# Performance work log

Hardware: AMD Instinct MI355X
Metric: run time of the kernel (lower is better)

## Reference

```python
import jax, jax.numpy as jnp
import numpy as np
from jax import lax

D_MODEL = 192
D_STATE = 16
D_CONV = 4
EXPAND = 2
D_INNER = D_MODEL * EXPAND           # 384
DT_RANK = (D_MODEL + 15) // 16       # 12
B, H, W = 4, 32, 32
N = H * W                            # 1024


def layernorm(x, g, b, eps=1e-5):
    m = x.mean(-1, keepdims=True)
    v = ((x - m) ** 2).mean(-1, keepdims=True)
    return (x - m) / jnp.sqrt(v + eps) * g + b


def mamba(u, Win, cw, cb, Wxp, Wdt, bdt, Alog, Dp, Wout):
    """mamba-ssm Mamba block. u: (B, L, d_model)."""
    Bb, L, _ = u.shape
    xz = u @ Win.T                                  # (B,L,2*d_inner)
    xh, z = jnp.split(xz, 2, axis=-1)
    # causal depthwise conv1d
    xc = xh.transpose(0, 2, 1)                      # (B,d_inner,L)
    xc = lax.conv_general_dilated(
        xc, cw[:, None, :], (1,), [(D_CONV - 1, 0)],
        feature_group_count=D_INNER,
        dimension_numbers=('NCH', 'OIH', 'NCH')) + cb[None, :, None]
    xs = jax.nn.silu(xc).transpose(0, 2, 1)         # (B,L,d_inner)
    dbl = xs @ Wxp.T                                # (B,L,dt_rank+2*d_state)
    dt = dbl[..., :DT_RANK]
    Bm = dbl[..., DT_RANK:DT_RANK + D_STATE]
    Cm = dbl[..., DT_RANK + D_STATE:]
    dt = jax.nn.softplus(dt @ Wdt.T + bdt)          # (B,L,d_inner)
    A = -jnp.exp(Alog)                              # (d_inner,d_state)

    def step(h, inp):
        dt_t, B_t, C_t, x_t = inp                   # (B,di),(B,ds),(B,ds),(B,di)
        dA = jnp.exp(dt_t[..., None] * A)           # (B,di,ds)
        h = dA * h + dt_t[..., None] * B_t[:, None, :] * x_t[..., None]
        return h, jnp.einsum('bds,bs->bd', h, C_t)

    h0 = jnp.zeros((Bb, D_INNER, D_STATE), u.dtype)
    _, ys = lax.scan(step, h0, (dt.transpose(1, 0, 2), Bm.transpose(1, 0, 2),
                                Cm.transpose(1, 0, 2), xs.transpose(1, 0, 2)))
    y = ys.transpose(1, 0, 2) + xs * Dp
    y = y * jax.nn.silu(z)
    return y @ Wout.T


mamba4 = jax.vmap(mamba)  # batched over the 4 scan directions


def to_col(x):    # row-major -> column-major sequence order
    return x.reshape(-1, H, W, D_MODEL).transpose(0, 2, 1, 3).reshape(-1, N, D_MODEL)


def from_col(x):  # inverse of to_col
    return x.reshape(-1, W, H, D_MODEL).transpose(0, 2, 1, 3).reshape(-1, N, D_MODEL)


def setup_inputs() -> dict:
    key = jax.random.key(0)
    ks = iter(jax.random.split(key, 32))
    s = 0.02
    d, di, ds, r = D_MODEL, D_INNER, D_STATE, DT_RANK
    inp = {}
    inp['x'] = jax.random.normal(next(ks), (B, d, H, W), jnp.float32)
    inp['norm_g'] = jnp.ones((d,), jnp.float32)
    inp['norm_b'] = jnp.zeros((d,), jnp.float32)
    inp['in_w'] = jax.random.normal(next(ks), (d, d), jnp.float32) * s
    inp['in_b'] = jnp.zeros((d,), jnp.float32)
    # 4 stacked Mamba blocks
    inp['m_in_w'] = jax.random.normal(next(ks), (4, 2 * di, d), jnp.float32) * s
    inp['m_conv_w'] = jax.random.normal(next(ks), (4, di, D_CONV), jnp.float32) * s
    inp['m_conv_b'] = jnp.zeros((4, di), jnp.float32)
    inp['m_xp_w'] = jax.random.normal(next(ks), (4, r + 2 * ds, di), jnp.float32) * s
    inp['m_dt_w'] = jax.random.normal(next(ks), (4, di, r), jnp.float32) * s
    inp['m_dt_b'] = jax.random.normal(next(ks), (4, di), jnp.float32) * 0.1 - 4.0
    inp['m_Alog'] = jnp.log(jnp.tile(jnp.arange(1, ds + 1, dtype=jnp.float32), (4, di, 1)))
    inp['m_D'] = jnp.ones((4, di), jnp.float32)
    inp['m_out_w'] = jax.random.normal(next(ks), (4, d, di), jnp.float32) * s
    # fusion MLP
    inp['f_w1'] = jax.random.normal(next(ks), (2 * d, 4 * d), jnp.float32) * s
    inp['f_b1'] = jnp.zeros((2 * d,), jnp.float32)
    inp['f_w2'] = jax.random.normal(next(ks), (d, 2 * d), jnp.float32) * s
    inp['f_b2'] = jnp.zeros((d,), jnp.float32)
    inp['o_w'] = jax.random.normal(next(ks), (d, d), jnp.float32) * s
    inp['o_b'] = jnp.zeros((d,), jnp.float32)
    inp['on_g'] = jnp.ones((d,), jnp.float32)
    inp['on_b'] = jnp.zeros((d,), jnp.float32)
    return inp


def reference(x, norm_g, norm_b, in_w, in_b, m_in_w, m_conv_w, m_conv_b,
              m_xp_w, m_dt_w, m_dt_b, m_Alog, m_D, m_out_w,
              f_w1, f_b1, f_w2, f_b2, o_w, o_b, on_g, on_b):
    xs = x.reshape(B, D_MODEL, N).transpose(0, 2, 1)     # b c h w -> b (hw) c
    xs = layernorm(xs, norm_g, norm_b)
    xp = xs @ in_w.T + in_b
    col = to_col(xp)
    seqs = jnp.stack([xp, jnp.flip(xp, 1), col, jnp.flip(col, 1)], 0)  # (4,B,N,C)
    ys = mamba4(seqs, m_in_w, m_conv_w, m_conv_b, m_xp_w, m_dt_w, m_dt_b,
                m_Alog, m_D, m_out_w)
    o0 = ys[0]
    o1 = jnp.flip(ys[1], 1)
    o2 = from_col(ys[2])
    o3 = from_col(jnp.flip(ys[3], 1))
    fused = jnp.concatenate([o0, o1, o2, o3], -1)        # (B,N,4C)
    hdn = jax.nn.gelu(fused @ f_w1.T + f_b1, approximate=False)
    hdn = hdn @ f_w2.T + f_b2
    out = hdn @ o_w.T + o_b
    out = layernorm(out, on_g, on_b) + xs
    return out.transpose(0, 2, 1).reshape(B, D_MODEL, H, W)
```

## Files before the change

kernel.cpp:

```cpp
#include <hip/hip_runtime.h>
#include <cstddef>

#define DM 192
#define DI 384
#define DS 16
#define DR 12
#define L 1024
#define ROWS 4096
#define SEG 32
#define ST  32

typedef unsigned short ushortx;
typedef short bf16x8 __attribute__((ext_vector_type(8)));
typedef float f32x4  __attribute__((ext_vector_type(4)));

__device__ __forceinline__ float wave_sum(float v) {
  #pragma unroll
  for (int off = 32; off > 0; off >>= 1) v += __shfl_xor(v, off);
  return v;
}

__device__ __forceinline__ ushortx f2bf(float x) {
  unsigned u = __float_as_uint(x);
  u += 0x7fffu + ((u >> 16) & 1u);
  return (ushortx)(u >> 16);
}
__device__ __forceinline__ float bf2f(ushortx u) {
  return __uint_as_float(((unsigned)u) << 16);
}

__device__ __forceinline__ int map_row(int t, int mode) {
  switch (mode) {
    case 1: return 1023 - t;
    case 2: return ((t & 31) << 5) | (t >> 5);
    case 3: { int u = 1023 - t; return ((u & 31) << 5) | (u >> 5); }
    case 4: return 1023 - (((t & 31) << 5) | (t >> 5));
    default: return t;
  }
}

struct WcvtArgs {
  const float* src[6];
  unsigned int off[6];
  unsigned int n[6];
};
__global__ __launch_bounds__(256) void prep_kernel(
    WcvtArgs a, ushortx* __restrict__ dst,
    const float* __restrict__ in_w, unsigned int_off,
    const float* __restrict__ in_b, float* __restrict__ bC,
    const float* __restrict__ x, const float* __restrict__ g,
    const float* __restrict__ b, float* __restrict__ xs, ushortx* __restrict__ xs_bf)
{
  int y = blockIdx.y;
  if (y < 6) {
    int i = (blockIdx.x * 256 + threadIdx.x) * 4;
    if (i < (int)a.n[y]) {
      float4 v = *(const float4*)(a.src[y] + i);
      ushort4 o;
      o.x = f2bf(v.x); o.y = f2bf(v.y); o.z = f2bf(v.z); o.w = f2bf(v.w);
      *(ushort4*)(dst + a.off[y] + i) = o;
    }
    return;
  }
  if (y == 6) {
    int i = blockIdx.x * 256 + threadIdx.x;
    if (i < DM * DM) {
      int n = i / DM, j = i % DM;
      dst[int_off + i] = f2bf(in_w[(size_t)j * DM + n]);
    }
    return;
  }
  if (y == 8) {
    int idx = blockIdx.x * 256 + threadIdx.x;
    if (idx < 4 * 768) {
      int k = idx / 768, n = idx % 768;
      const float* wr = a.src[0] + (size_t)k * 768 * DM + (size_t)n * DM;
      float acc = 0.f;
      for (int j = 0; j < DM; ++j) acc = fmaf(wr[j], in_b[j], acc);
      bC[idx] = acc;
    }
    return;
  }
  if (blockIdx.x >= 1024) return;
  int wave = threadIdx.x >> 6;
  int lane = threadIdx.x & 63;
  int r = blockIdx.x * 4 + wave;
  int bb = r >> 10, n = r & 1023;
  const float* xb = x + (size_t)bb * DM * L + n;
  float v[3];
  float s = 0.f, s2 = 0.f;
  #pragma unroll
  for (int j = 0; j < 3; ++j) {
    int c = lane + j * 64;
    v[j] = xb[(size_t)c * L];
    s += v[j]; s2 += v[j] * v[j];
  }
  s = wave_sum(s); s2 = wave_sum(s2);
  float mean = s * (1.f / DM);
  float var  = s2 * (1.f / DM) - mean * mean;
  float rstd = rsqrtf(var + 1e-5f);
  float* xo = xs + (size_t)r * DM;
  ushortx* xob = xs_bf + (size_t)r * DM;
  #pragma unroll
  for (int j = 0; j < 3; ++j) {
    int c = lane + j * 64;
    float val = (v[j] - mean) * rstd * g[c] + b[c];
    xo[c] = val;
    xob[c] = f2bf(val);
  }
}

template <int NIT>
__global__ __launch_bounds__(256) void gemm_fullk_kernel(
    const ushortx* __restrict__ A, int lda, const ushortx* __restrict__ W,
    const float* __restrict__ bias, ushortx* __restrict__ Cb,
    int ldc, int coff, int4 perm,
    long astride, long wstride, long cstride, int coffstride, int bstride)
{
  __shared__ __align__(16) short As[2][64][40];
  __shared__ __align__(16) short Bs[2][64][40];

  int z = blockIdx.z;
  A += (size_t)z * astride;
  W += (size_t)z * wstride;
  Cb += (size_t)z * cstride;
  if (bias) bias += (size_t)z * bstride;
  int permMode = (z == 0) ? perm.x : (z == 1) ? perm.y : (z == 2) ? perm.z : perm.w;
  int co = coff + z * coffstride;
  const int K = NIT * 32;

  int tid = threadIdx.x;
  int m0 = blockIdx.x * 64;
  int n0 = blockIdx.y * 64;

  int ar = tid >> 2, ak = (tid & 3) * 8;
  int arow = m0 + ar;
  int amrow = (arow & ~1023) | map_row(arow & 1023, permMode);
  const ushortx* ap = A + (size_t)amrow * lda + ak;
  const ushortx* wp = W + (size_t)(n0 + ar) * K + ak;

  int lane = tid & 63;
  int w = tid >> 6, wm = w >> 1, wn = w & 1;
  int lm = lane & 15, lq = lane >> 4;

  bf16x8 rA[NIT], rB[NIT];
  #pragma unroll
  for (int ki = 0; ki < NIT; ++ki) rA[ki] = *(const bf16x8*)(ap + ki * 32);
  #pragma unroll
  for (int ki = 0; ki < NIT; ++ki) rB[ki] = *(const bf16x8*)(wp + ki * 32);

  f32x4 acc[2][2];
  #pragma unroll
  for (int i = 0; i < 2; ++i)
    #pragma unroll
    for (int j = 0; j < 2; ++j) acc[i][j] = (f32x4){0.f, 0.f, 0.f, 0.f};

  *(bf16x8*)&As[0][ar][ak] = rA[0];
  *(bf16x8*)&Bs[0][ar][ak] = rB[0];
  __syncthreads();

  #pragma unroll
  for (int ki = 0; ki < NIT; ++ki) {
    int cur = ki & 1;
    bf16x8 fa[2], fb[2];
    #pragma unroll
    for (int i = 0; i < 2; ++i)
      fa[i] = *(const bf16x8*)&As[cur][wm * 32 + i * 16 + lm][lq * 8];
    #pragma unroll
    for (int j = 0; j < 2; ++j)
      fb[j] = *(const bf16x8*)&Bs[cur][wn * 32 + j * 16 + lm][lq * 8];
    #pragma unroll
    for (int i = 0; i < 2; ++i)
      #pragma unroll
      for (int j = 0; j < 2; ++j)
        acc[i][j] = __builtin_amdgcn_mfma_f32_16x16x32_bf16(fa[i], fb[j], acc[i][j], 0, 0, 0);
    if (ki + 1 < NIT) {
      int nxt = cur ^ 1;
      *(bf16x8*)&As[nxt][ar][ak] = rA[ki + 1];
      *(bf16x8*)&Bs[nxt][ar][ak] = rB[ki + 1];
      __syncthreads();
    }
  }

  #pragma unroll
  for (int i = 0; i < 2; ++i) {
    #pragma unroll
    for (int r = 0; r < 4; ++r) {
      int row = m0 + wm * 32 + i * 16 + lq * 4 + r;
      #pragma unroll
      for (int j = 0; j < 2; ++j) {
        int n = n0 + wn * 32 + j * 16 + lm;
        float v = acc[i][j][r];
        if (bias) v += bias[n];
        Cb[(size_t)row * ldc + co + n] = f2bf(v);
      }
    }
  }
}

template <int BM, int BN>
__global__ __launch_bounds__(256) void gemm_kernel(
    const ushortx* __restrict__ A, int lda, const ushortx* __restrict__ W,
    const float* __restrict__ bias, float* __restrict__ C, ushortx* __restrict__ Cb,
    int N, int K, int ldc, int coff, int4 perm, int act,
    long astride, long wstride, long cstride, int coffstride, int bstride)
{
  constexpr int MF = BM / 32;
  constexpr int NF = BN / 32;
  constexpr int AR = (BM * 32) / (256 * 8);
  constexpr int BR = (BN * 32) / (256 * 8);
  __shared__ __align__(16) short As[2][BM][40];
  __shared__ __align__(16) short Bs[2][BN][40];

  int z = blockIdx.z;
  A += (size_t)z * astride;
  W += (size_t)z * wstride;
  if (C)  C  += (size_t)z * cstride;
  if (Cb) Cb += (size_t)z * cstride;
  if (bias) bias += (size_t)z * bstride;
  int permMode = (z == 0) ? perm.x : (z == 1) ? perm.y : (z == 2) ? perm.z : perm.w;
  int co = coff + z * coffstride;

  int tid = threadIdx.x;
  int m0 = blockIdx.x * BM;
  int n0 = blockIdx.y * BN;

  int ar, ak;
  if (AR == 2) { ar = tid >> 1; ak = (tid & 1) * 16; }
  else         { ar = tid >> 2; ak = (tid & 3) * 8; }
  int arow = m0 + ar;
  int amrow = (arow & ~1023) | map_row(arow & 1023, permMode);
  const ushortx* ap = A + (size_t)amrow * lda + ak;

  int bn, bk;
  if (BR == 2) { bn = tid >> 1; bk = (tid & 1) * 16; }
  else         { bn = tid >> 2; bk = (tid & 3) * 8; }
  const ushortx* wp = W + (size_t)(n0 + bn) * K + bk;
  bool bok = (n0 + bn) < N;

  int lane = tid & 63;
  int w = tid >> 6, wm = w >> 1, wn = w & 1;
  int lm = lane & 15, lq = lane >> 4;

  f32x4 acc[MF][NF];
  #pragma unroll
  for (int i = 0; i < MF; ++i)
    #pragma unroll
    for (int j = 0; j < NF; ++j) acc[i][j] = (f32x4){0.f, 0.f, 0.f, 0.f};

  const bf16x8 zz = {0, 0, 0, 0, 0, 0, 0, 0};
  bf16x8 ra[AR], rb[BR];

  #pragma unroll
  for (int u = 0; u < AR; ++u) ra[u] = *(const bf16x8*)(ap + u * 8);
  #pragma unroll
  for (int u = 0; u < BR; ++u) rb[u] = bok ? *(const bf16x8*)(wp + u * 8) : zz;
  #pragma unroll
  for (int u = 0; u < AR; ++u) *(bf16x8*)&As[0][ar][ak + u * 8] = ra[u];
  #pragma unroll
  for (int u = 0; u < BR; ++u) *(bf16x8*)&Bs[0][bn][bk + u * 8] = rb[u];
  __syncthreads();

  int niter = K >> 5;
  for (int ki = 0; ki < niter; ++ki) {
    int cur = ki & 1;
    if (ki + 1 < niter) {
      int k0 = (ki + 1) * 32;
      #pragma unroll
      for (int u = 0; u < AR; ++u) ra[u] = *(const bf16x8*)(ap + k0 + u * 8);
      #pragma unroll
      for (int u = 0; u < BR; ++u) rb[u] = bok ? *(const bf16x8*)(wp + k0 + u * 8) : zz;
    }
    bf16x8 fa[MF], fb[NF];
    #pragma unroll
    for (int i = 0; i < MF; ++i)
      fa[i] = *(const bf16x8*)&As[cur][wm * (BM / 2) + i * 16 + lm][lq * 8];
    #pragma unroll
    for (int j = 0; j < NF; ++j)
      fb[j] = *(const bf16x8*)&Bs[cur][wn * (BN / 2) + j * 16 + lm][lq * 8];
    #pragma unroll
    for (int i = 0; i < MF; ++i)
      #pragma unroll
      for (int j = 0; j < NF; ++j)
        acc[i][j] = __builtin_amdgcn_mfma_f32_16x16x32_bf16(fa[i], fb[j], acc[i][j], 0, 0, 0);
    if (ki + 1 < niter) {
      int nxt = cur ^ 1;
      #pragma unroll
      for (int u = 0; u < AR; ++u) *(bf16x8*)&As[nxt][ar][ak + u * 8] = ra[u];
      #pragma unroll
      for (int u = 0; u < BR; ++u) *(bf16x8*)&Bs[nxt][bn][bk + u * 8] = rb[u];
      __syncthreads();
    }
  }

  #pragma unroll
  for (int i = 0; i < MF; ++i) {
    #pragma unroll
    for (int r = 0; r < 4; ++r) {
      int row = m0 + wm * (BM / 2) + i * 16 + lq * 4 + r;
      #pragma unroll
      for (int j = 0; j < NF; ++j) {
        int n = n0 + wn * (BN / 2) + j * 16 + lm;
        if (n < N) {
          float v = acc[i][j][r];
          if (bias) v += bias[n];
          if (act == 1) v = 0.5f * v * (1.f + erff(v * 0.70710678118f));
          if (C)  C [(size_t)row * ldc + co + n] = v;
          if (Cb) Cb[(size_t)row * ldc + co + n] = f2bf(v);
        }
      }
    }
  }
}

__global__ __launch_bounds__(256) void gemm_ln_kernel(
    const ushortx* __restrict__ A, const ushortx* __restrict__ W,
    const float* __restrict__ ob, const float* __restrict__ g,
    const float* __restrict__ b, const float* __restrict__ xs,
    float* __restrict__ out)
{
  __shared__ __align__(16) char smem[64 * 200 * 4];
  short* As0 = (short*)smem;
  short* As1 = As0 + 64 * 40;
  short* Bs0 = As1 + 64 * 40;
  short* Bs1 = Bs0 + 192 * 40;
  float* Ct  = (float*)smem;

  int tid = threadIdx.x;
  int m0 = blockIdx.x * 64;

  int ar = tid >> 2, ak = (tid & 3) * 8;
  const ushortx* ap = A + (size_t)(m0 + ar) * DM + ak;

  int lane = tid & 63;
  int w = tid >> 6, wm = w >> 1, wn = w & 1;
  int lm = lane & 15, lq = lane >> 4;

  f32x4 acc[2][6];
  #pragma unroll
  for (int i = 0; i < 2; ++i)
    #pragma unroll
    for (int j = 0; j < 6; ++j) acc[i][j] = (f32x4){0.f, 0.f, 0.f, 0.f};

  bf16x8 ra, rb[3];
  ra = *(const bf16x8*)ap;
  #pragma unroll
  for (int u = 0; u < 3; ++u) {
    int c = tid + u * 256;
    rb[u] = *(const bf16x8*)(W + (size_t)(c >> 2) * DM + (c & 3) * 8);
  }
  *(bf16x8*)&As0[ar * 40 + ak] = ra;
  #pragma unroll
  for (int u = 0; u < 3; ++u) {
    int c = tid + u * 256;
    *(bf16x8*)&Bs0[(c >> 2) * 40 + (c & 3) * 8] = rb[u];
  }
  __syncthreads();

  const int niter = DM / 32;
  for (int ki = 0; ki < niter; ++ki) {
    short* Ac = (ki & 1) ? As1 : As0;
    short* Bc = (ki & 1) ? Bs1 : Bs0;
    if (ki + 1 < niter) {
      int k0 = (ki + 1) * 32;
      ra = *(const bf16x8*)(ap + k0);
      #pragma unroll
      for (int u = 0; u < 3; ++u) {
        int c = tid + u * 256;
        rb[u] = *(const bf16x8*)(W + (size_t)(c >> 2) * DM + (c & 3) * 8 + k0);
      }
    }
    bf16x8 fa[2], fb[6];
    #pragma unroll
    for (int i = 0; i < 2; ++i)
      fa[i] = *(const bf16x8*)&Ac[(wm * 32 + i * 16 + lm) * 40 + lq * 8];
    #pragma unroll
    for (int j = 0; j < 6; ++j)
      fb[j] = *(const bf16x8*)&Bc[(wn * 96 + j * 16 + lm) * 40 + lq * 8];
    #pragma unroll
    for (int i = 0; i < 2; ++i)
      #pragma unroll
      for (int j = 0; j < 6; ++j)
        acc[i][j] = __builtin_amdgcn_mfma_f32_16x16x32_bf16(fa[i], fb[j], acc[i][j], 0, 0, 0);
    if (ki + 1 < niter) {
      short* An = (ki & 1) ? As0 : As1;
      short* Bn = (ki & 1) ? Bs0 : Bs1;
      *(bf16x8*)&An[ar * 40 + ak] = ra;
      #pragma unroll
      for (int u = 0; u < 3; ++u) {
        int c = tid + u * 256;
        *(bf16x8*)&Bn[(c >> 2) * 40 + (c & 3) * 8] = rb[u];
      }
    }
    __syncthreads();
  }

  #pragma unroll
  for (int i = 0; i < 2; ++i) {
    #pragma unroll
    for (int r = 0; r < 4; ++r) {
      int row = wm * 32 + i * 16 + lq * 4 + r;
      #pragma unroll
      for (int j = 0; j < 6; ++j) {
        int col = wn * 96 + j * 16 + lm;
        Ct[row * 200 + col] = acc[i][j][r] + ob[col];
      }
    }
  }
  __syncthreads();

  int row = tid >> 2, p = tid & 3;
  const float* base = Ct + row * 200 + p * 48;
  float s = 0.f, s2 = 0.f;
  #pragma unroll
  for (int c = 0; c < 48; ++c) { float v = base[c]; s += v; s2 += v * v; }
  s  += __shfl_xor(s, 1);  s  += __shfl_xor(s, 2);
  s2 += __shfl_xor(s2, 1); s2 += __shfl_xor(s2, 2);
  float mean = s * (1.f / DM);
  float var  = s2 * (1.f / DM) - mean * mean;
  float rstd = rsqrtf(var + 1e-5f);
  int gr = m0 + row, bb = gr >> 10, n = gr & 1023;
  const float* xsr = xs + (size_t)gr * DM + p * 48;
  float* op = out + (size_t)bb * DM * L + n;
  #pragma unroll
  for (int c48 = 0; c48 < 48; ++c48) {
    int c = p * 48 + c48;
    float val = (base[c48] - mean) * rstd * g[c] + b[c] + xsr[c48];
    op[(size_t)c * L] = val;
  }
}

__global__ __launch_bounds__(256) void conv_silu_kernel(
    const ushortx* __restrict__ xz, const float* __restrict__ cw,
    const float* __restrict__ cb, ushortx* __restrict__ xsm_bf)
{
  int idx = blockIdx.x * 256 + threadIdx.x;
  int d = idx % DI;
  int rest = idx / DI;
  int tq = rest & 255;
  int seq = rest >> 8;
  int k = seq >> 2;
  int t0 = tq * 4;
  const ushortx* xh = xz + (size_t)seq * L * (2 * DI) + d;
  const float* w = cw + ((size_t)k * DI + d) * 4;
  float w0 = w[0], w1 = w[1], w2 = w[2], w3 = w[3];
  float bias = cb[k * DI + d];
  float in[7];
  #pragma unroll
  for (int j = 0; j < 7; ++j) {
    int t = t0 - 3 + j;
    in[j] = (t >= 0) ? bf2f(xh[(size_t)t * (2 * DI)]) : 0.f;
  }
  ushortx* yo = xsm_bf + ((size_t)seq * L + t0) * DI + d;
  #pragma unroll
  for (int i = 0; i < 4; ++i) {
    float acc = bias;
    acc = fmaf(w0, in[i],     acc);
    acc = fmaf(w1, in[i + 1], acc);
    acc = fmaf(w2, in[i + 2], acc);
    acc = fmaf(w3, in[i + 3], acc);
    float sig = 1.f / (1.f + __expf(-acc));
    yo[(size_t)i * DI] = f2bf(acc * sig);
  }
}

__global__ __launch_bounds__(256) void dt_kernel(
    const float* __restrict__ dbl, const float* __restrict__ Wdt,
    const float* __restrict__ bdt, ushortx* __restrict__ dt)
{
  int idx = blockIdx.x * 256 + threadIdx.x;
  int d = idx % DI;
  int row = idx / DI;
  int k = row >> 12;
  const float* dl = dbl + (size_t)row * 44;
  const float* w = Wdt + ((size_t)k * DI + d) * DR;
  float acc = bdt[k * DI + d];
  #pragma unroll
  for (int r = 0; r < DR; ++r) acc = fmaf(w[r], dl[r], acc);
  float v = (acc > 20.f) ? acc : log1pf(__expf(acc));
  dt[idx] = f2bf(v);
}

__global__ __launch_bounds__(64) void scan_pass1(
    const float* __restrict__ dbl, const ushortx* __restrict__ dt,
    const ushortx* __restrict__ xsm_bf, const float* __restrict__ Alog,
    float* __restrict__ hseg, float* __restrict__ Sseg)
{
  __shared__ __align__(16) float sB[ST][16];
  int seq = blockIdx.y, g = blockIdx.z, k = seq >> 2;
  int d = blockIdx.x * 64 + threadIdx.x;

  const float* bbase = dbl + ((size_t)seq * L + g * ST) * 44 + 12;
  #pragma unroll
  for (int j = 0; j < 2; ++j) {
    int i = threadIdx.x + j * 64;
    int t = i >> 2, q = (i & 3) * 4;
    *(float4*)&sB[t][q] = *(const float4*)(bbase + (size_t)t * 44 + q);
  }
  float A[16];
  const float* alp = Alog + ((size_t)k * DI + d) * DS;
  #pragma unroll
  for (int s = 0; s < 16; ++s) A[s] = -__expf(alp[s]);

  const ushortx* dtp = dt     + ((size_t)seq * L + g * ST) * DI + d;
  const ushortx* xp  = xsm_bf + ((size_t)seq * L + g * ST) * DI + d;
  __syncthreads();

  float h[16];
  #pragma unroll
  for (int s = 0; s < 16; ++s) h[s] = 0.f;
  float sdt = 0.f;
  float rDt[4], rX[4];
  #pragma unroll
  for (int j = 0; j < 4; ++j) {
    rDt[j] = bf2f(dtp[(size_t)j * DI]);
    rX [j] = bf2f(xp [(size_t)j * DI]);
  }

  #pragma unroll 4
  for (int t = 0; t < ST; ++t) {
    float dtv = rDt[t & 3], xv = rX[t & 3];
    if (t + 4 < ST) {
      rDt[t & 3] = bf2f(dtp[(size_t)(t + 4) * DI]);
      rX [t & 3] = bf2f(xp [(size_t)(t + 4) * DI]);
    }
    float dtx = dtv * xv;
    sdt += dtv;
    #pragma unroll
    for (int s = 0; s < 16; ++s) {
      float dA = __expf(dtv * A[s]);
      h[s] = fmaf(dA, h[s], dtx * sB[t][s]);
    }
  }
  float* hp = hseg + (((size_t)seq * SEG + g) * DI + d) * DS;
  #pragma unroll
  for (int s = 0; s < 16; ++s) hp[s] = h[s];
  Sseg[((size_t)seq * SEG + g) * DI + d] = sdt;
}

__global__ __launch_bounds__(64) void scan_mid(
    float* __restrict__ hseg, const float* __restrict__ Sseg,
    const float* __restrict__ Alog)
{
  int seq = blockIdx.y, k = seq >> 2;
  int d = blockIdx.x * 64 + threadIdx.x;
  float A[16];
  const float* alp = Alog + ((size_t)k * DI + d) * DS;
  #pragma unroll
  for (int s = 0; s < 16; ++s) A[s] = -__expf(alp[s]);
  float h[16];
  #pragma unroll
  for (int s = 0; s < 16; ++s) h[s] = 0.f;
  for (int g = 0; g < SEG; ++g) {
    float* hp = hseg + (((size_t)seq * SEG + g) * DI + d) * DS;
    float Sg = Sseg[((size_t)seq * SEG + g) * DI + d];
    float tmp[16];
    #pragma unroll
    for (int s = 0; s < 16; ++s) tmp[s] = hp[s];
    #pragma unroll
    for (int s = 0; s < 16; ++s) hp[s] = h[s];
    #pragma unroll
    for (int s = 0; s < 16; ++s)
      h[s] = fmaf(h[s], __expf(A[s] * Sg), tmp[s]);
  }
}

__global__ __launch_bounds__(64) void scan_pass2(
    const float* __restrict__ dbl, const ushortx* __restrict__ dt,
    const ushortx* __restrict__ xz,
    ushortx* __restrict__ xy,
    const float* __restrict__ Alog, const float* __restrict__ Dp,
    const float* __restrict__ hseg)
{
  __shared__ __align__(16) float sBC[ST][32];
  int seq = blockIdx.y, g = blockIdx.z, k = seq >> 2;
  int d = blockIdx.x * 64 + threadIdx.x;

  const float* bcbase = dbl + ((size_t)seq * L + g * ST) * 44 + 12;
  #pragma unroll
  for (int j = 0; j < 4; ++j) {
    int i = threadIdx.x + j * 64;
    int t = i >> 3, q = (i & 7) * 4;
    *(float4*)&sBC[t][q] = *(const float4*)(bcbase + (size_t)t * 44 + q);
  }
  float A[16];
  const float* alp = Alog + ((size_t)k * DI + d) * DS;
  #pragma unroll
  for (int s = 0; s < 16; ++s) A[s] = -__expf(alp[s]);
  float Dv = Dp[k * DI + d];

  float h[16];
  {
    const float* hp = hseg + (((size_t)seq * SEG + g) * DI + d) * DS;
    #pragma unroll
    for (int s = 0; s < 16; ++s) h[s] = hp[s];
  }

  const ushortx* dtp = dt + ((size_t)seq * L + g * ST) * DI + d;
  const ushortx* zp  = xz + ((size_t)seq * L + g * ST) * (2 * DI) + DI + d;
  ushortx*       yp  = xy + ((size_t)seq * L + g * ST) * DI + d;
  __syncthreads();

  float rDt[4], rX[4], rZ[4];
  #pragma unroll
  for (int j = 0; j < 4; ++j) {
    rDt[j] = bf2f(dtp[(size_t)j * DI]);
    rX [j] = bf2f(yp [(size_t)j * DI]);
    rZ [j] = bf2f(zp [(size_t)j * (2 * DI)]);
  }

  #pragma unroll 4
  for (int t = 0; t < ST; ++t) {
    float dtv = rDt[t & 3], xv = rX[t & 3], zv = rZ[t & 3];
    if (t + 4 < ST) {
      rDt[t & 3] = bf2f(dtp[(size_t)(t + 4) * DI]);
      rX [t & 3] = bf2f(yp [(size_t)(t + 4) * DI]);
      rZ [t & 3] = bf2f(zp [(size_t)(t + 4) * (2 * DI)]);
    }
    float dtx = dtv * xv;
    float y = 0.f;
    #pragma unroll
    for (int s = 0; s < 16; ++s) {
      float dA = __expf(dtv * A[s]);
      h[s] = fmaf(dA, h[s], dtx * sBC[t][s]);
      y = fmaf(h[s], sBC[t][16 + s], y);
    }
    y = fmaf(Dv, xv, y);
    float sig = 1.f / (1.f + __expf(-zv));
    yp[(size_t)t * DI] = f2bf(y * (zv * sig));
  }
}

template <int BM, int BN>
static inline void gemm(const ushortx* A, int lda, const ushortx* W, const float* bias,
                        float* C, ushortx* Cb,
                        int N, int K, int ldc, int coff, int4 perm, int act,
                        int nz, long astride, long wstride, long cstride, int coffstride,
                        hipStream_t s, int M = ROWS, int bstride = 0) {
  dim3 grid(M / BM, (N + BN - 1) / BN, nz);
  gemm_kernel<BM, BN><<<grid, 256, 0, s>>>(A, lda, W, bias, C, Cb, N, K, ldc, coff, perm, act,
                                           astride, wstride, cstride, coffstride, bstride);
}

extern "C" void kernel_launch(void* const* d_in, const int* in_sizes, int n_in,
                              void* d_out, int out_size, void* d_ws, size_t ws_size,
                              hipStream_t stream) {
  (void)in_sizes; (void)n_in; (void)out_size; (void)ws_size;
  const float* x        = (const float*)d_in[0];
  const float* norm_g   = (const float*)d_in[1];
  const float* norm_b   = (const float*)d_in[2];
  const float* in_w     = (const float*)d_in[3];
  const float* in_b     = (const float*)d_in[4];
  const float* m_in_w   = (const float*)d_in[5];
  const float* m_conv_w = (const float*)d_in[6];
  const float* m_conv_b = (const float*)d_in[7];
  const float* m_xp_w   = (const float*)d_in[8];
  const float* m_dt_w   = (const float*)d_in[9];
  const float* m_dt_b   = (const float*)d_in[10];
  const float* m_Alog   = (const float*)d_in[11];
  const float* m_D      = (const float*)d_in[12];
  const float* m_out_w  = (const float*)d_in[13];
  const float* f_w1     = (const float*)d_in[14];
  const float* f_b1     = (const float*)d_in[15];
  const float* f_w2     = (const float*)d_in[16];
  const float* f_b2     = (const float*)d_in[17];
  const float* o_w      = (const float*)d_in[18];
  const float* o_b      = (const float*)d_in[19];
  const float* on_g     = (const float*)d_in[20];
  const float* on_b     = (const float*)d_in[21];
  float* out = (float*)d_out;

  float* ws   = (float*)d_ws;
  float* xs   = ws;
  float* dbl  = xs + 786432;
  float* hseg = dbl + 720896;
  float* Sseg = hseg + 3145728;
  float* bC   = Sseg + 196608;
  ushortx* xs_bf  = (ushortx*)(bC + 4096);
  ushortx* wbf    = xs_bf + 786432;
  ushortx* WinC   = wbf + 1394688;
  ushortx* dt_bf  = WinC + 589824;
  ushortx* xz_bf  = dt_bf + 6291456;
  ushortx* xsm_bf = xz_bf + 12582912;
  ushortx* fused_bf = xz_bf;
  ushortx* hdn_bf   = fused_bf + 3145728;
  ushortx* h2_bf    = hdn_bf + 1572864;

  const unsigned W_MIN = 0, W_XP = 589824, W_OUT = 657408, W_F1 = 952320,
                 W_F2 = 1247232, W_O = 1320960, W_INT = 1357824;

  int4 p0 = make_int4(0, 0, 0, 0);
  int4 pfwd = make_int4(0, 1, 2, 3);
  int4 pinv = make_int4(0, 1, 2, 4);

  {
    WcvtArgs a;
    a.src[0] = m_in_w;  a.off[0] = W_MIN; a.n[0] = 589824;
    a.src[1] = m_xp_w;  a.off[1] = W_XP;  a.n[1] = 67584;
    a.src[2] = m_out_w; a.off[2] = W_OUT; a.n[2] = 294912;
    a.src[3] = f_w1;    a.off[3] = W_F1;  a.n[3] = 294912;
    a.src[4] = f_w2;    a.off[4] = W_F2;  a.n[4] = 73728;
    a.src[5] = o_w;     a.off[5] = W_O;   a.n[5] = 36864;
    prep_kernel<<<dim3(1024, 9), 256, 0, stream>>>(
        a, wbf, in_w, W_INT, in_b, bC, x, norm_g, norm_b, xs, xs_bf);
  }
  gemm<64, 64>(wbf + W_MIN, DM, wbf + W_INT, nullptr, nullptr, WinC,
               DM, DM, DM, 0, p0, 0, 4, (long)768 * DM, 0, (long)768 * DM, 0,
               stream, 768);
  gemm_fullk_kernel<6><<<dim3(ROWS / 64, 768 / 64, 4), 256, 0, stream>>>(
      xs_bf, DM, WinC, bC, xz_bf, 2 * DI, 0, pfwd,
      0, (long)768 * DM, (long)ROWS * 2 * DI, 0, 768);
  conv_silu_kernel<<<(16 * 256 * DI) / 256, 256, 0, stream>>>(xz_bf, m_conv_w, m_conv_b, xsm_bf);
  gemm<64, 64>(xsm_bf, DI, wbf + W_XP, nullptr, dbl, nullptr, 44, DI, 44, 0, p0, 0,
               4, (long)ROWS * DI, (long)44 * DI, (long)ROWS * 44, 0, stream);
  dt_kernel<<<(16 * L * DI) / 256, 256, 0, stream>>>(dbl, m_dt_w, m_dt_b, dt_bf);
  scan_pass1<<<dim3(DI / 64, 16, SEG), 64, 0, stream>>>(dbl, dt_bf, xsm_bf, m_Alog, hseg, Sseg);
  scan_mid<<<dim3(DI / 64, 16), 64, 0, stream>>>(hseg, Sseg, m_Alog);
  scan_pass2<<<dim3(DI / 64, 16, SEG), 64, 0, stream>>>(dbl, dt_bf, xz_bf, xsm_bf,
                                                        m_Alog, m_D, hseg);
  gemm_fullk_kernel<12><<<dim3(ROWS / 64, DM / 64, 4), 256, 0, stream>>>(
      xsm_bf, DI, wbf + W_OUT, nullptr, fused_bf, 4 * DM, 0, pinv,
      (long)ROWS * DI, (long)DM * DI, 0, DM, 0);
  gemm<64, 64>(fused_bf, 4 * DM, wbf + W_F1, f_b1, nullptr, hdn_bf, 2 * DM, 4 * DM, 2 * DM,
               0, p0, 1, 1, 0, 0, 0, 0, stream);
  gemm_fullk_kernel<12><<<dim3(ROWS / 64, DM / 64, 1), 256, 0, stream>>>(
      hdn_bf, 2 * DM, wbf + W_F2, f_b2, h2_bf, DM, 0, p0,
      0, 0, 0, 0, 0);
  gemm_ln_kernel<<<64, 256, 0, stream>>>(h2_bf, wbf + W_O, o_b, on_g, on_b, xs, out);
}
```

Before: 298.3 us.

## Fuse dt projection into scan passes, parallelize scan_mid, shrink gemm_ln tiles

Removes the separate dt_kernel and recomputes the dt projection plus softplus inside both scan passes from the dbl rows staged in shared memory. This avoids writing and twice re-reading a bf16 dt tensor of 16x1024x384 elements, at the cost of twelve extra FMAs and a softplus per step in each pass. scan_mid is rewritten to assign one thread per (d, state) pair with prefetched loads, which raises parallelism for the serial segment combine. gemm_ln_kernel now uses 16-row tiles, giving 256 blocks instead of 64 and better GPU occupancy, though it re-reads the weight tile more often.

Result: slower. 311.1 us (+4.3%).

```diff
diff --git a/kernel.cpp b/kernel.cpp
--- a/kernel.cpp
+++ b/kernel.cpp
@@ -319,113 +319,102 @@
     const float* __restrict__ b, const float* __restrict__ xs,
     float* __restrict__ out)
 {
-  __shared__ __align__(16) char smem[64 * 200 * 4];
-  short* As0 = (short*)smem;
-  short* As1 = As0 + 64 * 40;
-  short* Bs0 = As1 + 64 * 40;
-  short* Bs1 = Bs0 + 192 * 40;
-  float* Ct  = (float*)smem;
+  __shared__ __align__(16) short As[2][16][40];
+  __shared__ __align__(16) short Bs[2][192][40];
+  __shared__ float Ct[16][200];
 
   int tid = threadIdx.x;
-  int m0 = blockIdx.x * 64;
-
-  int ar = tid >> 2, ak = (tid & 3) * 8;
+  int m0 = blockIdx.x * 16;
+
+  bool aok = tid < 64;
+  int ar = (tid >> 2) & 15, ak = (tid & 3) * 8;
   const ushortx* ap = A + (size_t)(m0 + ar) * DM + ak;
 
   int lane = tid & 63;
-  int w = tid >> 6, wm = w >> 1, wn = w & 1;
+  int w = tid >> 6;
   int lm = lane & 15, lq = lane >> 4;
 
-  f32x4 acc[2][6];
-  #pragma unroll
-  for (int i = 0; i < 2; ++i)
-    #pragma unroll
-    for (int j = 0; j < 6; ++j) acc[i][j] = (f32x4){0.f, 0.f, 0.f, 0.f};
+  f32x4 acc[3];
+  #pragma unroll
+  for (int j = 0; j < 3; ++j) acc[j] = (f32x4){0.f, 0.f, 0.f, 0.f};
 
   bf16x8 ra, rb[3];
-  ra = *(const bf16x8*)ap;
+  if (aok) ra = *(const bf16x8*)ap;
   #pragma unroll
   for (int u = 0; u < 3; ++u) {
     int c = tid + u * 256;
     rb[u] = *(const bf16x8*)(W + (size_t)(c >> 2) * DM + (c & 3) * 8);
   }
-  *(bf16x8*)&As0[ar * 40 + ak] = ra;
+  if (aok) *(bf16x8*)&As[0][ar][ak] = ra;
   #pragma unroll
   for (int u = 0; u < 3; ++u) {
     int c = tid + u * 256;
-    *(bf16x8*)&Bs0[(c >> 2) * 40 + (c & 3) * 8] = rb[u];
+    *(bf16x8*)&Bs[0][c >> 2][(c & 3) * 8] = rb[u];
   }
   __syncthreads();
 
   const int niter = DM / 32;
   for (int ki = 0; ki < niter; ++ki) {
-    short* Ac = (ki & 1) ? As1 : As0;
-    short* Bc = (ki & 1) ? Bs1 : Bs0;
+    int cur = ki & 1;
     if (ki + 1 < niter) {
       int k0 = (ki + 1) * 32;
-      ra = *(const bf16x8*)(ap + k0);
+      if (aok) ra = *(const bf16x8*)(ap + k0);
       #pragma unroll
       for (int u = 0; u < 3; ++u) {
         int c = tid + u * 256;
         rb[u] = *(const bf16x8*)(W + (size_t)(c >> 2) * DM + (c & 3) * 8 + k0);
       }
     }
-    bf16x8 fa[2], fb[6];
-    #pragma unroll
-    for (int i = 0; i < 2; ++i)
-      fa[i] = *(const bf16x8*)&Ac[(wm * 32 + i * 16 + lm) * 40 + lq * 8];
-    #pragma unroll
-    for (int j = 0; j < 6; ++j)
-      fb[j] = *(const bf16x8*)&Bc[(wn * 96 + j * 16 + lm) * 40 + lq * 8];
-    #pragma unroll
-    for (int i = 0; i < 2; ++i)
-      #pragma unroll
-      for (int j = 0; j < 6; ++j)
-        acc[i][j] = __builtin_amdgcn_mfma_f32_16x16x32_bf16(fa[i], fb[j], acc[i][j], 0, 0, 0);
+    bf16x8 fa = *(const bf16x8*)&As[cur][lm][lq * 8];
+    bf16x8 fb[3];
+    #pragma unroll
+    for (int j = 0; j < 3; ++j)
+      fb[j] = *(const bf16x8*)&Bs[cur][w * 48 + j * 16 + lm][lq * 8];
+    #pragma unroll
+    for (int j = 0; j < 3; ++j)
+      acc[j] = __builtin_amdgcn_mfma_f32_16x16x32_bf16(fa, fb[j], acc[j], 0, 0, 0);
     if (ki + 1 < niter) {
-      short* An = (ki & 1) ? As0 : As1;
-      short* Bn = (ki & 1) ? Bs0 : Bs1;
-      *(bf16x8*)&An[ar * 40 + ak] = ra;
+      int nxt = cur ^ 1;
+      if (aok) *(bf16x8*)&As[nxt][ar][ak] = ra;
       #pragma unroll
       for (int u = 0; u < 3; ++u) {
         int c = tid + u * 256;
-        *(bf16x8*)&Bn[(c >> 2) * 40 + (c & 3) * 8] = rb[u];
+        *(bf16x8*)&Bs[nxt][c >> 2][(c & 3) * 8] = rb[u];
       }
-    }
-    __syncthreads();
-  }
-
-  #pragma unroll
-  for (int i = 0; i < 2; ++i) {
-    #pragma unroll
-    for (int r = 0; r < 4; ++r) {
-      int row = wm * 32 + i * 16 + lq * 4 + r;
-      #pragma unroll
-      for (int j = 0; j < 6; ++j) {
-        int col = wn * 96 + j * 16 + lm;
-        Ct[row * 200 + col] = acc[i][j][r] + ob[col];
-      }
+      __syncthreads();
+    }
+  }
+
+  #pragma unroll
+  for (int r = 0; r < 4; ++r) {
+    int row = lq * 4 + r;
+    #pragma unroll
+    for (int j = 0; j < 3; ++j) {
+      int col = w * 48 + j * 16 + lm;
+      Ct[row][col] = acc[j][r] + ob[col];
     }
   }
   __syncthreads();
 
-  int row = tid >> 2, p = tid & 3;
-  const float* base = Ct + row * 200 + p * 48;
+  int row = tid >> 4, p = tid & 15;
+  const float* base = &Ct[row][0] + p * 12;
   float s = 0.f, s2 = 0.f;
   #pragma unroll
-  for (int c = 0; c < 48; ++c) { float v = base[c]; s += v; s2 += v * v; }
+  for (int c = 0; c < 12; ++c) { float v = base[c]; s += v; s2 += v * v; }
   s  += __shfl_xor(s, 1);  s  += __shfl_xor(s, 2);
+  s  += __shfl_xor(s, 4);  s  += __shfl_xor(s, 8);
   s2 += __shfl_xor(s2, 1); s2 += __shfl_xor(s2, 2);
+  s2 += __shfl_xor(s2, 4); s2 += __shfl_xor(s2, 8);
   float mean = s * (1.f / DM);
   float var  = s2 * (1.f / DM) - mean * mean;
   float rstd = rsqrtf(var + 1e-5f);
   int gr = m0 + row, bb = gr >> 10, n = gr & 1023;
-  const float* xsr = xs + (size_t)gr * DM + p * 48;
+  const float* xsr = xs + (size_t)gr * DM + p * 12;
   float* op = out + (size_t)bb * DM * L + n;
   #pragma unroll
-  for (int c48 = 0; c48 < 48; ++c48) {
-    int c = p * 48 + c48;
-    float val = (base[c48] - mean) * rstd * g[c] + b[c] + xsr[c48];
+  for (int c12 = 0; c12 < 12; ++c12) {
+    int c = p * 12 + c12;
+    float val = (base[c12] - mean) * rstd * g[c] + b[c] + xsr[c12];
     op[(size_t)c * L] = val;
   }
 }
@@ -464,72 +453,74 @@
   }
 }
 
-__global__ __launch_bounds__(256) void dt_kernel(
-    const float* __restrict__ dbl, const float* __restrict__ Wdt,
-    const float* __restrict__ bdt, ushortx* __restrict__ dt)
-{
-  int idx = blockIdx.x * 256 + threadIdx.x;
-  int d = idx % DI;
-  int row = idx / DI;
-  int k = row >> 12;
-  const float* dl = dbl + (size_t)row * 44;
-  const float* w = Wdt + ((size_t)k * DI + d) * DR;
-  float acc = bdt[k * DI + d];
-  #pragma unroll
-  for (int r = 0; r < DR; ++r) acc = fmaf(w[r], dl[r], acc);
-  float v = (acc > 20.f) ? acc : log1pf(__expf(acc));
-  dt[idx] = f2bf(v);
+__device__ __forceinline__ float dt_inline(const float* __restrict__ row,
+                                           const float wdt[12], float bdt_v) {
+  float a0 = fmaf(wdt[0], row[0], bdt_v);
+  float a1 = wdt[1] * row[1];
+  float a2 = wdt[2] * row[2];
+  float a3 = wdt[3] * row[3];
+  #pragma unroll
+  for (int r = 4; r < 12; r += 4) {
+    a0 = fmaf(wdt[r],     row[r],     a0);
+    a1 = fmaf(wdt[r + 1], row[r + 1], a1);
+    a2 = fmaf(wdt[r + 2], row[r + 2], a2);
+    a3 = fmaf(wdt[r + 3], row[r + 3], a3);
+  }
+  float acc = (a0 + a1) + (a2 + a3);
+  return (acc > 20.f) ? acc : log1pf(__expf(acc));
 }
 
 __global__ __launch_bounds__(64) void scan_pass1(
-    const float* __restrict__ dbl, const ushortx* __restrict__ dt,
-    const ushortx* __restrict__ xsm_bf, const float* __restrict__ Alog,
+    const float* __restrict__ dbl, const ushortx* __restrict__ xsm_bf,
+    const float* __restrict__ Alog, const float* __restrict__ Wdt,
+    const float* __restrict__ bdt,
     float* __restrict__ hseg, float* __restrict__ Sseg)
 {
-  __shared__ __align__(16) float sB[ST][16];
+  __shared__ __align__(16) float sB[ST][28];
   int seq = blockIdx.y, g = blockIdx.z, k = seq >> 2;
   int d = blockIdx.x * 64 + threadIdx.x;
 
-  const float* bbase = dbl + ((size_t)seq * L + g * ST) * 44 + 12;
-  #pragma unroll
-  for (int j = 0; j < 2; ++j) {
+  const float* bbase = dbl + ((size_t)seq * L + g * ST) * 44;
+  #pragma unroll
+  for (int j = 0; j < 4; ++j) {
     int i = threadIdx.x + j * 64;
-    int t = i >> 2, q = (i & 3) * 4;
-    *(float4*)&sB[t][q] = *(const float4*)(bbase + (size_t)t * 44 + q);
+    if (i < 224) {
+      int t = i / 7, q = (i % 7) * 4;
+      *(float4*)&sB[t][q] = *(const float4*)(bbase + (size_t)t * 44 + q);
+    }
   }
   float A[16];
   const float* alp = Alog + ((size_t)k * DI + d) * DS;
   #pragma unroll
   for (int s = 0; s < 16; ++s) A[s] = -__expf(alp[s]);
-
-  const ushortx* dtp = dt     + ((size_t)seq * L + g * ST) * DI + d;
-  const ushortx* xp  = xsm_bf + ((size_t)seq * L + g * ST) * DI + d;
+  float wdt[12];
+  const float* wpt = Wdt + ((size_t)k * DI + d) * DR;
+  #pragma unroll
+  for (int r = 0; r < DR; ++r) wdt[r] = wpt[r];
+  float bdt_v = bdt[k * DI + d];
+
+  const ushortx* xp = xsm_bf + ((size_t)seq * L + g * ST) * DI + d;
   __syncthreads();
 
   float h[16];
   #pragma unroll
   for (int s = 0; s < 16; ++s) h[s] = 0.f;
   float sdt = 0.f;
-  float rDt[4], rX[4];
-  #pragma unroll
-  for (int j = 0; j < 4; ++j) {
-    rDt[j] = bf2f(dtp[(size_t)j * DI]);
-    rX [j] = bf2f(xp [(size_t)j * DI]);
-  }
+  float rX[4];
+  #pragma unroll
+  for (int j = 0; j < 4; ++j) rX[j] = bf2f(xp[(size_t)j * DI]);
 
   #pragma unroll 4
   for (int t = 0; t < ST; ++t) {
-    float dtv = rDt[t & 3], xv = rX[t & 3];
-    if (t + 4 < ST) {
-      rDt[t & 3] = bf2f(dtp[(size_t)(t + 4) * DI]);
-      rX [t & 3] = bf2f(xp [(size_t)(t + 4) * DI]);
-    }
+    float xv = rX[t & 3];
+    if (t + 4 < ST) rX[t & 3] = bf2f(xp[(size_t)(t + 4) * DI]);
+    float dtv = dt_inline(&sB[t][0], wdt, bdt_v);
     float dtx = dtv * xv;
     sdt += dtv;
     #pragma unroll
     for (int s = 0; s < 16; ++s) {
       float dA = __expf(dtv * A[s]);
-      h[s] = fmaf(dA, h[s], dtx * sB[t][s]);
+      h[s] = fmaf(dA, h[s], dtx * sB[t][12 + s]);
     }
   }
   float* hp = hseg + (((size_t)seq * SEG + g) * DI + d) * DS;
@@ -543,50 +534,62 @@
     const float* __restrict__ Alog)
 {
   int seq = blockIdx.y, k = seq >> 2;
+  int tid = threadIdx.x;
+  int d = blockIdx.x * 4 + (tid >> 4);
+  int s = tid & 15;
+  float A = -__expf(Alog[((size_t)k * DI + d) * DS + s]);
+
+  float* hb = hseg + ((size_t)seq * SEG * DI + d) * DS + s;
+  const float* Sb = Sseg + (size_t)seq * SEG * DI + d;
+
+  float rH[4], rS[4];
+  #pragma unroll
+  for (int j = 0; j < 4; ++j) {
+    rH[j] = hb[(size_t)j * DI * DS];
+    rS[j] = Sb[(size_t)j * DI];
+  }
+  float h = 0.f;
+  #pragma unroll 4
+  for (int g = 0; g < SEG; ++g) {
+    float hv = rH[g & 3], Sg = rS[g & 3];
+    if (g + 4 < SEG) {
+      rH[g & 3] = hb[(size_t)(g + 4) * DI * DS];
+      rS[g & 3] = Sb[(size_t)(g + 4) * DI];
+    }
+    hb[(size_t)g * DI * DS] = h;
+    h = fmaf(h, __expf(A * Sg), hv);
+  }
+}
+
+__global__ __launch_bounds__(64) void scan_pass2(
+    const float* __restrict__ dbl, const ushortx* __restrict__ xz,
+    ushortx* __restrict__ xy,
+    const float* __restrict__ Alog, const float* __restrict__ Dp,
+    const float* __restrict__ hseg, const float* __restrict__ Wdt,
+    const float* __restrict__ bdt)
+{
+  __shared__ __align__(16) float sBC[ST][44];
+  int seq = blockIdx.y, g = blockIdx.z, k = seq >> 2;
   int d = blockIdx.x * 64 + threadIdx.x;
+
+  const float* bcbase = dbl + ((size_t)seq * L + g * ST) * 44;
+  #pragma unroll
+  for (int j = 0; j < 6; ++j) {
+    int i = threadIdx.x + j * 64;
+    if (i < 352) {
+      int t = i / 11, q = (i % 11) * 4;
+      *(float4*)&sBC[t][q] = *(const float4*)(bcbase + (size_t)t * 44 + q);
+    }
+  }
   float A[16];
   const float* alp = Alog + ((size_t)k * DI + d) * DS;
   #pragma unroll
   for (int s = 0; s < 16; ++s) A[s] = -__expf(alp[s]);
-  float h[16];
-  #pragma unroll
-  for (int s = 0; s < 16; ++s) h[s] = 0.f;
-  for (int g = 0; g < SEG; ++g) {
-    float* hp = hseg + (((size_t)seq * SEG + g) * DI + d) * DS;
-    float Sg = Sseg[((size_t)seq * SEG + g) * DI + d];
-    float tmp[16];
-    #pragma unroll
-    for (int s = 0; s < 16; ++s) tmp[s] = hp[s];
-    #pragma unroll
-    for (int s = 0; s < 16; ++s) hp[s] = h[s];
-    #pragma unroll
-    for (int s = 0; s < 16; ++s)
-      h[s] = fmaf(h[s], __expf(A[s] * Sg), tmp[s]);
-  }
-}
-
-__global__ __launch_bounds__(64) void scan_pass2(
-    const float* __restrict__ dbl, const ushortx* __restrict__ dt,
-    const ushortx* __restrict__ xz,
-    ushortx* __restrict__ xy,
-    const float* __restrict__ Alog, const float* __restrict__ Dp,
-    const float* __restrict__ hseg)
-{
-  __shared__ __align__(16) float sBC[ST][32];
-  int seq = blockIdx.y, g = blockIdx.z, k = seq >> 2;
-  int d = blockIdx.x * 64 + threadIdx.x;
-
-  const float* bcbase = dbl + ((size_t)seq * L + g * ST) * 44 + 12;
-  #pragma unroll
-  for (int j = 0; j < 4; ++j) {
-    int i = threadIdx.x + j * 64;
-    int t = i >> 3, q = (i & 7) * 4;
-    *(float4*)&sBC[t][q] = *(const float4*)(bcbase + (size_t)t * 44 + q);
-  }
-  float A[16];
-  const float* alp = Alog + ((size_t)k * DI + d) * DS;
-  #pragma unroll
-  for (int s = 0; s < 16; ++s) A[s] = -__expf(alp[s]);
+  float wdt[12];
+  const float* wpt = Wdt + ((size_t)k * DI + d) * DR;
+  #pragma unroll
+  for (int r = 0; r < DR; ++r) wdt[r] = wpt[r];
+  float bdt_v = bdt[k * DI + d];
   float Dv = Dp[k * DI + d];
 
   float h[16];
@@ -596,34 +599,32 @@
     for (int s = 0; s < 16; ++s) h[s] = hp[s];
   }
 
-  const ushortx* dtp = dt + ((size_t)seq * L + g * ST) * DI + d;
   const ushortx* zp  = xz + ((size_t)seq * L + g * ST) * (2 * DI) + DI + d;
   ushortx*       yp  = xy + ((size_t)seq * L + g * ST) * DI + d;
   __syncthreads();
 
-  float rDt[4], rX[4], rZ[4];
+  float rX[4], rZ[4];
   #pragma unroll
   for (int j = 0; j < 4; ++j) {
-    rDt[j] = bf2f(dtp[(size_t)j * DI]);
-    rX [j] = bf2f(yp [(size_t)j * DI]);
-    rZ [j] = bf2f(zp [(size_t)j * (2 * DI)]);
+    rX[j] = bf2f(yp[(size_t)j * DI]);
+    rZ[j] = bf2f(zp[(size_t)j * (2 * DI)]);
   }
 
   #pragma unroll 4
   for (int t = 0; t < ST; ++t) {
-    float dtv = rDt[t & 3], xv = rX[t & 3], zv = rZ[t & 3];
+    float xv = rX[t & 3], zv = rZ[t & 3];
     if (t + 4 < ST) {
-      rDt[t & 3] = bf2f(dtp[(size_t)(t + 4) * DI]);
-      rX [t & 3] = bf2f(yp [(size_t)(t + 4) * DI]);
-      rZ [t & 3] = bf2f(zp [(size_t)(t + 4) * (2 * DI)]);
-    }
+      rX[t & 3] = bf2f(yp[(size_t)(t + 4) * DI]);
+      rZ[t & 3] = bf2f(zp[(size_t)(t + 4) * (2 * DI)]);
+    }
+    float dtv = dt_inline(&sBC[t][0], wdt, bdt_v);
     float dtx = dtv * xv;
     float y = 0.f;
     #pragma unroll
     for (int s = 0; s < 16; ++s) {
       float dA = __expf(dtv * A[s]);
-      h[s] = fmaf(dA, h[s], dtx * sBC[t][s]);
-      y = fmaf(h[s], sBC[t][16 + s], y);
+      h[s] = fmaf(dA, h[s], dtx * sBC[t][12 + s]);
+      y = fmaf(h[s], sBC[t][28 + s], y);
     }
     y = fmaf(Dv, xv, y);
     float sig = 1.f / (1.f + __expf(-zv));
@@ -713,11 +714,11 @@
   conv_silu_kernel<<<(16 * 256 * DI) / 256, 256, 0, stream>>>(xz_bf, m_conv_w, m_conv_b, xsm_bf);
   gemm<64, 64>(xsm_bf, DI, wbf + W_XP, nullptr, dbl, nullptr, 44, DI, 44, 0, p0, 0,
                4, (long)ROWS * DI, (long)44 * DI, (long)ROWS * 44, 0, stream);
-  dt_kernel<<<(16 * L * DI) / 256, 256, 0, stream>>>(dbl, m_dt_w, m_dt_b, dt_bf);
-  scan_pass1<<<dim3(DI / 64, 16, SEG), 64, 0, stream>>>(dbl, dt_bf, xsm_bf, m_Alog, hseg, Sseg);
-  scan_mid<<<dim3(DI / 64, 16), 64, 0, stream>>>(hseg, Sseg, m_Alog);
-  scan_pass2<<<dim3(DI / 64, 16, SEG), 64, 0, stream>>>(dbl, dt_bf, xz_bf, xsm_bf,
-                                                        m_Alog, m_D, hseg);
+  scan_pass1<<<dim3(DI / 64, 16, SEG), 64, 0, stream>>>(dbl, xsm_bf, m_Alog,
+                                                        m_dt_w, m_dt_b, hseg, Sseg);
+  scan_mid<<<dim3(DI / 4, 16), 64, 0, stream>>>(hseg, Sseg, m_Alog);
+  scan_pass2<<<dim3(DI / 64, 16, SEG), 64, 0, stream>>>(dbl, xz_bf, xsm_bf,
+                                                        m_Alog, m_D, hseg, m_dt_w, m_dt_b);
   gemm_fullk_kernel<12><<<dim3(ROWS / 64, DM / 64, 4), 256, 0, stream>>>(
       xsm_bf, DI, wbf + W_OUT, nullptr, fused_bf, 4 * DM, 0, pinv,
       (long)ROWS * DI, (long)DM * DI, 0, DM, 0);
@@ -726,5 +727,5 @@
   gemm_fullk_kernel<12><<<dim3(ROWS / 64, DM / 64, 1), 256, 0, stream>>>(
       hdn_bf, 2 * DM, wbf + W_F2, f_b2, h2_bf, DM, 0, p0,
       0, 0, 0, 0, 0);
-  gemm_ln_kernel<<<64, 256, 0, stream>>>(h2_bf, wbf + W_O, o_b, on_g, on_b, xs, out);
-}
+  gemm_ln_kernel<<<ROWS / 16, 256, 0, stream>>>(h2_bf, wbf + W_O, o_b, on_g, on_b, xs, out);
+}
```
